# Optimization experiments

Measured on AMD Instinct MI355X. Metric: run time of the kernel, lower is better.

## Reference

```python
import jax, jax.numpy as jnp
import numpy as np

N = 50000       # nodes
E = 800000      # edges
H = 128         # hidden_channels
L = 5           # num_layers
EIN = 16        # edge_in_channels
G = 512         # graphs in batch
NODE_VOCAB = 100
BN_EPS = 1e-5


def setup_inputs() -> dict:
    key = jax.random.key(0)
    ks = jax.random.split(key, 12)
    s = 0.1  # init scale
    return {
        "x": jax.random.randint(ks[0], (N,), 0, NODE_VOCAB, dtype=jnp.int32),
        "edge_index": jax.random.randint(ks[1], (2, E), 0, N, dtype=jnp.int32),
        "edge_attr": jax.random.normal(ks[2], (E, EIN), jnp.float32),
        "batch": jnp.sort(jax.random.randint(ks[3], (N,), 0, G, dtype=jnp.int32)),
        "node_emb": jax.random.normal(ks[4], (NODE_VOCAB, H), jnp.float32) * s,
        "edge_W": jax.random.normal(ks[5], (L, EIN, H), jnp.float32) * s,
        "edge_b": jnp.zeros((L, H), jnp.float32),
        "eps": jnp.zeros((L,), jnp.float32),
        "W1": jax.random.normal(ks[6], (L, H, 2 * H), jnp.float32) * s,
        "b1": jnp.zeros((L, 2 * H), jnp.float32),
        "g1": jnp.ones((L, 2 * H), jnp.float32),
        "be1": jnp.zeros((L, 2 * H), jnp.float32),
        "W2": jax.random.normal(ks[7], (L, 2 * H, H), jnp.float32) * s,
        "b2": jnp.zeros((L, H), jnp.float32),
        "bn_g": jnp.ones((L, H), jnp.float32),
        "bn_b": jnp.zeros((L, H), jnp.float32),
        "out_W": jax.random.normal(ks[8], (H, H), jnp.float32) * s,
        "out_b": jnp.zeros((H,), jnp.float32),
    }


def _bn(h, gamma, beta):
    # training-mode BatchNorm1d: batch statistics over the node axis
    m = h.mean(0)
    v = jnp.mean((h - m) ** 2, axis=0)
    return (h - m) * jax.lax.rsqrt(v + BN_EPS) * gamma + beta


def reference(x, edge_index, edge_attr, batch, node_emb, edge_W, edge_b, eps,
              W1, b1, g1, be1, W2, b2, bn_g, bn_b, out_W, out_b):
    h = node_emb[x]                                   # [N,H] node encoder
    src, dst = edge_index[0], edge_index[1]
    for i in range(L):
        # EGINConv: edge encode, gather->relu->scatter-add, GIN MLP
        e = edge_attr @ edge_W[i] + edge_b[i]         # [E,H]
        msg = jax.nn.relu(h[src] + e)                 # gather + relu
        agg = jax.ops.segment_sum(msg, dst, num_segments=N)  # scatter-add
        z = (1.0 + eps[i]) * h + agg
        z = jax.nn.relu(_bn(z @ W1[i] + b1[i], g1[i], be1[i]))  # mlp inner
        h = _bn(z @ W2[i] + b2[i], bn_g[i], bn_b[i])  # inter-layer BN
        if i < L - 1:
            h = jax.nn.relu(h)                        # dropout: eval (identity)
    # global_mean_pool
    sums = jax.ops.segment_sum(h, batch, num_segments=G)
    cnt = jax.ops.segment_sum(jnp.ones((N, 1), h.dtype), batch, num_segments=G)
    pooled = sums / jnp.maximum(cnt, 1.0)
    return pooled @ out_W + out_b                     # [G,H]
```

## Files before the change

kernel.cpp:

```cpp
#include <hip/hip_runtime.h>
#include <hip/hip_fp16.h>

#define N_NODES 50000
#define N_EDGES 800000
#define HD 128
#define NLAYERS 5
#define EINC 16
#define NG 512

typedef _Float16 half8 __attribute__((ext_vector_type(8)));
typedef _Float16 half2v __attribute__((ext_vector_type(2)));
typedef float f32x4 __attribute__((ext_vector_type(4)));
typedef float f32x2 __attribute__((ext_vector_type(2)));

__global__ __launch_bounds__(256) void k_embed(const int* __restrict__ x,
                                               const float* __restrict__ emb,
                                               _Float16* __restrict__ h) {
  int i = blockIdx.x * 256 + threadIdx.x;
  if (i < N_NODES * 16) {
    int n = i >> 4, cv = i & 15;
    const float* src = &emb[(size_t)x[n] * HD + cv * 8];
    float4 a0 = *(const float4*)&src[0];
    float4 a1 = *(const float4*)&src[4];
    half8 p;
    p[0] = (_Float16)a0.x; p[1] = (_Float16)a0.y; p[2] = (_Float16)a0.z; p[3] = (_Float16)a0.w;
    p[4] = (_Float16)a1.x; p[5] = (_Float16)a1.y; p[6] = (_Float16)a1.z; p[7] = (_Float16)a1.w;
    *(half8*)&h[(size_t)n * HD + cv * 8] = p;
  }
}

__global__ __launch_bounds__(256) void k_hist(const int* __restrict__ ei,
                                              int* __restrict__ deg) {
  int e = blockIdx.x * 256 + threadIdx.x;
  if (e < N_EDGES) atomicAdd(&deg[ei[N_EDGES + e]], 1);
}

__global__ __launch_bounds__(256) void k_scan1(const int* __restrict__ deg,
                                               int* __restrict__ incl,
                                               int* __restrict__ bsum) {
  __shared__ int s[256];
  int i = blockIdx.x * 256 + threadIdx.x;
  int v = (i < N_NODES) ? deg[i] : 0;
  s[threadIdx.x] = v;
  __syncthreads();
  for (int d = 1; d < 256; d <<= 1) {
    int t = (threadIdx.x >= d) ? s[threadIdx.x - d] : 0;
    __syncthreads();
    s[threadIdx.x] += t;
    __syncthreads();
  }
  if (i < N_NODES) incl[i] = s[threadIdx.x];
  if (threadIdx.x == 255) bsum[blockIdx.x] = s[255];
}

__global__ void k_scan2(int* __restrict__ bsum, int nb) {
  __shared__ int s[256];
  int v = (threadIdx.x < nb) ? bsum[threadIdx.x] : 0;
  s[threadIdx.x] = v;
  __syncthreads();
  for (int d = 1; d < 256; d <<= 1) {
    int t = (threadIdx.x >= d) ? s[threadIdx.x - d] : 0;
    __syncthreads();
    s[threadIdx.x] += t;
    __syncthreads();
  }
  if (threadIdx.x < nb) bsum[threadIdx.x] = s[threadIdx.x];
}

__global__ __launch_bounds__(256) void k_scan3(const int* __restrict__ deg,
                                               const int* __restrict__ incl,
                                               const int* __restrict__ bsum,
                                               int* __restrict__ offs,
                                               int* __restrict__ cursor) {
  int i = blockIdx.x * 256 + threadIdx.x;
  if (i < N_NODES) {
    int base = (blockIdx.x > 0) ? bsum[blockIdx.x - 1] : 0;
    int start = base + incl[i] - deg[i];
    offs[i] = start;
    cursor[i] = start;
    if (i == N_NODES - 1) offs[N_NODES] = N_EDGES;
  }
}

__global__ __launch_bounds__(256) void k_scatter(const int* __restrict__ ei,
                                                 int* __restrict__ cursor,
                                                 int2* __restrict__ edata) {
  int e = blockIdx.x * 256 + threadIdx.x;
  if (e < N_EDGES) {
    int dst = ei[N_EDGES + e];
    int pos = atomicAdd(&cursor[dst], 1);
    edata[pos] = make_int2(ei[e], e);
  }
}

__global__ __launch_bounds__(256) void k_cvtw1(const float* __restrict__ W1,
                                               _Float16* __restrict__ w1t) {
  int i = blockIdx.x * 256 + threadIdx.x;
  if (i < NLAYERS * 256 * 128) {
    int l = i >> 15, r = i & 32767;
    int n = r >> 7, k = r & 127;
    w1t[i] = (_Float16)W1[(size_t)l * 32768 + k * 256 + n];
  }
}
__global__ __launch_bounds__(256) void k_cvtw2(const float* __restrict__ W2,
                                               _Float16* __restrict__ w2t) {
  int i = blockIdx.x * 256 + threadIdx.x;
  if (i < NLAYERS * 128 * 256) {
    int l = i >> 15, r = i & 32767;
    int n = r >> 8, k = r & 255;
    w2t[i] = (_Float16)W2[(size_t)l * 32768 + k * 128 + n];
  }
}

__global__ __launch_bounds__(256) void k_aggr(const int* __restrict__ offs,
                                              const int2* __restrict__ edata,
                                              const float* __restrict__ ea,
                                              const float* __restrict__ W,
                                              const float* __restrict__ eb,
                                              const float* __restrict__ epsA, int layer,
                                              const _Float16* __restrict__ hraw,
                                              const float* __restrict__ bnsc,
                                              const float* __restrict__ bnsh,
                                              int fuse_bn,
                                              _Float16* __restrict__ z) {
  const int wid = threadIdx.x >> 6;
  const int lane = threadIdx.x & 63;
  int n = blockIdx.x * 4 + wid;
  if (n >= N_NODES) return;
  const int c0 = lane * 2;

  f32x2 wp[EINC];
#pragma unroll
  for (int k = 0; k < EINC; ++k) wp[k] = *(const f32x2*)&W[k * HD + c0];
  const f32x2 ebp = *(const f32x2*)&eb[c0];
  const float epsv = 1.0f + epsA[layer];
  const f32x2 zero = {0.f, 0.f};
  f32x2 scp = {1.f, 1.f}, shp = {0.f, 0.f};
  if (fuse_bn) {
    scp = *(const f32x2*)&bnsc[c0];
    shp = *(const f32x2*)&bnsh[c0];
  }

  int j0 = offs[n], j1 = offs[n + 1];
  half2v hv = *(const half2v*)&hraw[(size_t)n * HD + c0];
  f32x2 hn; hn[0] = (float)hv[0]; hn[1] = (float)hv[1];
  if (fuse_bn) hn = __builtin_elementwise_max(__builtin_elementwise_fma(hn, scp, shp), zero);
  f32x2 acc;
  acc[0] = epsv * hn[0];
  acc[1] = epsv * hn[1];

  int j = j0;
  for (; j + 3 < j1; j += 4) {
    int2 d0 = edata[j], d1 = edata[j + 1], d2 = edata[j + 2], d3 = edata[j + 3];
    const float* r0 = &ea[(size_t)__builtin_amdgcn_readfirstlane(d0.y) * EINC];
    const float* r1 = &ea[(size_t)__builtin_amdgcn_readfirstlane(d1.y) * EINC];
    const float* r2 = &ea[(size_t)__builtin_amdgcn_readfirstlane(d2.y) * EINC];
    const float* r3 = &ea[(size_t)__builtin_amdgcn_readfirstlane(d3.y) * EINC];
    half2v v0h = *(const half2v*)&hraw[(size_t)d0.x * HD + c0];
    half2v v1h = *(const half2v*)&hraw[(size_t)d1.x * HD + c0];
    half2v v2h = *(const half2v*)&hraw[(size_t)d2.x * HD + c0];
    half2v v3h = *(const half2v*)&hraw[(size_t)d3.x * HD + c0];
    f32x2 g0, g1, g2, g3;
    g0[0] = (float)v0h[0]; g0[1] = (float)v0h[1];
    g1[0] = (float)v1h[0]; g1[1] = (float)v1h[1];
    g2[0] = (float)v2h[0]; g2[1] = (float)v2h[1];
    g3[0] = (float)v3h[0]; g3[1] = (float)v3h[1];
    if (fuse_bn) {
      g0 = __builtin_elementwise_max(__builtin_elementwise_fma(g0, scp, shp), zero);
      g1 = __builtin_elementwise_max(__builtin_elementwise_fma(g1, scp, shp), zero);
      g2 = __builtin_elementwise_max(__builtin_elementwise_fma(g2, scp, shp), zero);
      g3 = __builtin_elementwise_max(__builtin_elementwise_fma(g3, scp, shp), zero);
    }
    f32x2 e0 = ebp, e1 = ebp, e2 = ebp, e3 = ebp;
#pragma unroll
    for (int k = 0; k < EINC; ++k) {
      f32x2 w2 = wp[k];
      float a0 = r0[k], a1 = r1[k], a2 = r2[k], a3 = r3[k];
      f32x2 va0 = {a0, a0}, va1 = {a1, a1}, va2 = {a2, a2}, va3 = {a3, a3};
      e0 = __builtin_elementwise_fma(va0, w2, e0);
      e1 = __builtin_elementwise_fma(va1, w2, e1);
      e2 = __builtin_elementwise_fma(va2, w2, e2);
      e3 = __builtin_elementwise_fma(va3, w2, e3);
    }
    acc += __builtin_elementwise_max(g0 + e0, zero);
    acc += __builtin_elementwise_max(g1 + e1, zero);
    acc += __builtin_elementwise_max(g2 + e2, zero);
    acc += __builtin_elementwise_max(g3 + e3, zero);
  }
  for (; j < j1; ++j) {
    int2 d0 = edata[j];
    const float* r0 = &ea[(size_t)__builtin_amdgcn_readfirstlane(d0.y) * EINC];
    half2v v0h = *(const half2v*)&hraw[(size_t)d0.x * HD + c0];
    f32x2 g0; g0[0] = (float)v0h[0]; g0[1] = (float)v0h[1];
    if (fuse_bn) g0 = __builtin_elementwise_max(__builtin_elementwise_fma(g0, scp, shp), zero);
    f32x2 e0 = ebp;
#pragma unroll
    for (int k = 0; k < EINC; ++k) {
      float a0 = r0[k];
      f32x2 va0 = {a0, a0};
      e0 = __builtin_elementwise_fma(va0, wp[k], e0);
    }
    acc += __builtin_elementwise_max(g0 + e0, zero);
  }
  half2v oz; oz[0] = (_Float16)acc[0]; oz[1] = (_Float16)acc[1];
  *(half2v*)&z[(size_t)n * HD + c0] = oz;
}

__global__ __launch_bounds__(256) void k_gemm1m(const _Float16* __restrict__ z,
                                                const _Float16* __restrict__ w1t,
                                                const float* __restrict__ bias,
                                                _Float16* __restrict__ y1h,
                                                float* __restrict__ gsum,
                                                float* __restrict__ gsq) {
  __shared__ _Float16 sA[128 * 40];
  __shared__ _Float16 sBT[128 * 40];
  __shared__ float ssum[128], ssq[128];
  const int tid = threadIdx.x;
  const int lane = tid & 63;
  const int wid = tid >> 6;
  const int wm = wid >> 1, wn = wid & 1;
  const int m0 = blockIdx.x * 128;
  const int n0 = blockIdx.y * 128;

  if (tid < 128) { ssum[tid] = 0.f; ssq[tid] = 0.f; }

  f32x4 acc[4][4];
  const f32x4 zz = {0.f, 0.f, 0.f, 0.f};
#pragma unroll
  for (int a = 0; a < 4; ++a)
#pragma unroll
    for (int b = 0; b < 4; ++b) acc[a][b] = zz;

  const int srow = tid >> 1;
  const int skh = (tid & 1) * 16;

  for (int k0 = 0; k0 < 128; k0 += 32) {
    {
      int n = m0 + srow;
      half8 p0, p1;
      if (n < N_NODES) {
        p0 = *(const half8*)&z[(size_t)n * 128 + k0 + skh];
        p1 = *(const half8*)&z[(size_t)n * 128 + k0 + skh + 8];
      } else {
#pragma unroll
        for (int j = 0; j < 8; ++j) { p0[j] = (_Float16)0.f; p1[j] = (_Float16)0.f; }
      }
      *(half8*)&sA[srow * 40 + skh] = p0;
      *(half8*)&sA[srow * 40 + skh + 8] = p1;
    }
    {
      half8 u0 = *(const half8*)&w1t[(size_t)(n0 + srow) * 128 + k0 + skh];
      half8 u1 = *(const half8*)&w1t[(size_t)(n0 + srow) * 128 + k0 + skh + 8];
      *(half8*)&sBT[srow * 40 + skh] = u0;
      *(half8*)&sBT[srow * 40 + skh + 8] = u1;
    }
    __syncthreads();
    half8 af[4], bf[4];
#pragma unroll
    for (int t = 0; t < 4; ++t) {
      af[t] = *(const half8*)&sA[(wm * 64 + t * 16 + (lane & 15)) * 40 + (lane >> 4) * 8];
      bf[t] = *(const half8*)&sBT[(wn * 64 + t * 16 + (lane & 15)) * 40 + (lane >> 4) * 8];
    }
#pragma unroll
    for (int tm = 0; tm < 4; ++tm)
#pragma unroll
      for (int tn = 0; tn < 4; ++tn)
        acc[tm][tn] = __builtin_amdgcn_mfma_f32_16x16x32_f16(af[tm], bf[tn], acc[tm][tn], 0, 0, 0);
    __syncthreads();
  }

  float bsv[4];
#pragma unroll
  for (int tn = 0; tn < 4; ++tn) bsv[tn] = bias[n0 + wn * 64 + tn * 16 + (lane & 15)];
  float sacc[4] = {0.f, 0.f, 0.f, 0.f}, qacc[4] = {0.f, 0.f, 0.f, 0.f};
#pragma unroll
  for (int tm = 0; tm < 4; ++tm) {
    int nbase = m0 + wm * 64 + tm * 16 + (lane >> 4) * 4;
#pragma unroll
    for (int r = 0; r < 4; ++r) {
      int n = nbase + r;
      if (n < N_NODES) {
#pragma unroll
        for (int tn = 0; tn < 4; ++tn) {
          float v = acc[tm][tn][r] + bsv[tn];
          y1h[(size_t)n * 256 + n0 + wn * 64 + tn * 16 + (lane & 15)] = (_Float16)v;
          sacc[tn] += v; qacc[tn] += v * v;
        }
      }
    }
  }
#pragma unroll
  for (int tn = 0; tn < 4; ++tn) {
    int c = wn * 64 + tn * 16 + (lane & 15);
    atomicAdd(&ssum[c], sacc[tn]);
    atomicAdd(&ssq[c], qacc[tn]);
  }
  __syncthreads();
  if (tid < 128) {
    unsafeAtomicAdd(&gsum[n0 + tid], ssum[tid]);
    unsafeAtomicAdd(&gsq[n0 + tid], ssq[tid]);
  }
}

__global__ __launch_bounds__(256) void k_gemm2m(const _Float16* __restrict__ y1h,
                                                const float* __restrict__ sc,
                                                const float* __restrict__ sh,
                                                const _Float16* __restrict__ w2t,
                                                const float* __restrict__ bias,
                                                _Float16* __restrict__ y2,
                                                float* __restrict__ gsum,
                                                float* __restrict__ gsq) {
  __shared__ _Float16 sA[64 * 40];
  __shared__ _Float16 sBT[128 * 40];
  __shared__ float ssc[256], ssh[256];
  __shared__ float ssum[128], ssq[128];
  const int tid = threadIdx.x;
  const int lane = tid & 63;
  const int wid = tid >> 6;
  const int wm = wid >> 1, wn = wid & 1;
  const int m0 = blockIdx.x * 64;

  ssc[tid] = sc[tid];
  ssh[tid] = sh[tid];
  if (tid < 128) { ssum[tid] = 0.f; ssq[tid] = 0.f; }
  __syncthreads();

  f32x4 acc[2][4];
  const f32x4 zz = {0.f, 0.f, 0.f, 0.f};
#pragma unroll
  for (int a = 0; a < 2; ++a)
#pragma unroll
    for (int b = 0; b < 4; ++b) acc[a][b] = zz;

  const int arow = tid >> 2;
  const int akq = (tid & 3) * 8;
  const int brow = tid >> 1;
  const int bkh = (tid & 1) * 16;

  for (int k0 = 0; k0 < 256; k0 += 32) {
    {
      int n = m0 + arow;
      half8 p;
      if (n < N_NODES) {
        half8 yv = *(const half8*)&y1h[(size_t)n * 256 + k0 + akq];
#pragma unroll
        for (int j = 0; j < 8; ++j) {
          float v = fmaxf((float)yv[j] * ssc[k0 + akq + j] + ssh[k0 + akq + j], 0.f);
          p[j] = (_Float16)v;
        }
      } else {
#pragma unroll
        for (int j = 0; j < 8; ++j) p[j] = (_Float16)0.f;
      }
      *(half8*)&sA[arow * 40 + akq] = p;
    }
    {
      half8 u0 = *(const half8*)&w2t[(size_t)brow * 256 + k0 + bkh];
      half8 u1 = *(const half8*)&w2t[(size_t)brow * 256 + k0 + bkh + 8];
      *(half8*)&sBT[brow * 40 + bkh] = u0;
      *(half8*)&sBT[brow * 40 + bkh + 8] = u1;
    }
    __syncthreads();
    half8 af[2], bf[4];
#pragma unroll
    for (int t = 0; t < 2; ++t)
      af[t] = *(const half8*)&sA[(wm * 32 + t * 16 + (lane & 15)) * 40 + (lane >> 4) * 8];
#pragma unroll
    for (int t = 0; t < 4; ++t)
      bf[t] = *(const half8*)&sBT[(wn * 64 + t * 16 + (lane & 15)) * 40 + (lane >> 4) * 8];
#pragma unroll
    for (int tm = 0; tm < 2; ++tm)
#pragma unroll
      for (int tn = 0; tn < 4; ++tn)
        acc[tm][tn] = __builtin_amdgcn_mfma_f32_16x16x32_f16(af[tm], bf[tn], acc[tm][tn], 0, 0, 0);
    __syncthreads();
  }

  float bsv[4];
#pragma unroll
  for (int tn = 0; tn < 4; ++tn) bsv[tn] = bias[wn * 64 + tn * 16 + (lane & 15)];
  float sacc[4] = {0.f, 0.f, 0.f, 0.f}, qacc[4] = {0.f, 0.f, 0.f, 0.f};
#pragma unroll
  for (int tm = 0; tm < 2; ++tm) {
    int nbase = m0 + wm * 32 + tm * 16 + (lane >> 4) * 4;
#pragma unroll
    for (int r = 0; r < 4; ++r) {
      int n = nbase + r;
      if (n < N_NODES) {
#pragma unroll
        for (int tn = 0; tn < 4; ++tn) {
          float v = acc[tm][tn][r] + bsv[tn];
          y2[(size_t)n * 128 + wn * 64 + tn * 16 + (lane & 15)] = (_Float16)v;
          sacc[tn] += v; qacc[tn] += v * v;
        }
      }
    }
  }
#pragma unroll
  for (int tn = 0; tn < 4; ++tn) {
    int c = wn * 64 + tn * 16 + (lane & 15);
    atomicAdd(&ssum[c], sacc[tn]);
    atomicAdd(&ssq[c], qacc[tn]);
  }
  __syncthreads();
  if (tid < 128) {
    unsafeAtomicAdd(&gsum[tid], ssum[tid]);
    unsafeAtomicAdd(&gsq[tid], ssq[tid]);
  }
}

__global__ void k_bnfin(const float* __restrict__ sum, const float* __restrict__ sq,
                        const float* __restrict__ g, const float* __restrict__ b,
                        float* __restrict__ sc, float* __restrict__ sh, int C) {
  int c = blockIdx.x * blockDim.x + threadIdx.x;
  if (c < C) {
    const float invN = 1.0f / (float)N_NODES;
    float m = sum[c] * invN;
    float v = fmaxf(sq[c] * invN - m * m, 0.0f);
    float rs = rsqrtf(v + 1e-5f);
    float scale = g[c] * rs;
    sc[c] = scale;
    sh[c] = b[c] - m * scale;
  }
}

__global__ void k_goff(const int* __restrict__ batch, int* __restrict__ goff) {
  int g = blockIdx.x * blockDim.x + threadIdx.x;
  if (g <= NG) {
    if (g == NG) { goff[g] = N_NODES; return; }
    int lo = 0, hi = N_NODES;
    while (lo < hi) { int mid = (lo + hi) >> 1; if (batch[mid] < g) lo = mid + 1; else hi = mid; }
    goff[g] = lo;
  }
}

__global__ __launch_bounds__(256) void k_poolseg(const _Float16* __restrict__ y2raw,
                                                 const float* __restrict__ sc,
                                                 const float* __restrict__ sh,
                                                 const int* __restrict__ goff,
                                                 float* __restrict__ pooled) {
  __shared__ float sred[256];
  int g = blockIdx.x;
  int c = threadIdx.x & 127;
  int half = threadIdx.x >> 7;
  int n0 = goff[g], n1 = goff[g + 1];
  float s = 0.f;
  for (int n = n0 + half; n < n1; n += 2) s += (float)y2raw[(size_t)n * HD + c];
  sred[threadIdx.x] = s;
  __syncthreads();
  if (threadIdx.x < 128) {
    float tot = sred[threadIdx.x] + sred[threadIdx.x + 128];
    float cntf = fmaxf((float)(n1 - n0), 1.0f);
    pooled[g * HD + threadIdx.x] = sc[threadIdx.x] * (tot / cntf) + sh[threadIdx.x];
  }
}

__global__ __launch_bounds__(128) void k_final(const float* __restrict__ pooled,
                                               const float* __restrict__ oW,
                                               const float* __restrict__ ob,
                                               float* __restrict__ out) {
  __shared__ float sP[HD];
  int g = blockIdx.x;
  int c = threadIdx.x;
  sP[c] = pooled[g * HD + c];
  __syncthreads();
  float acc = ob[c];
#pragma unroll 8
  for (int k = 0; k < HD; ++k) acc += sP[k] * oW[k * HD + c];
  out[g * HD + c] = acc;
}

extern "C" void kernel_launch(void* const* d_in, const int* in_sizes, int n_in,
                              void* d_out, int out_size, void* d_ws, size_t ws_size,
                              hipStream_t stream) {
  const int* x = (const int*)d_in[0];
  const int* ei = (const int*)d_in[1];
  const float* ea = (const float*)d_in[2];
  const int* batch = (const int*)d_in[3];
  const float* emb = (const float*)d_in[4];
  const float* eW = (const float*)d_in[5];
  const float* eb = (const float*)d_in[6];
  const float* epsA = (const float*)d_in[7];
  const float* W1 = (const float*)d_in[8];
  const float* b1 = (const float*)d_in[9];
  const float* g1 = (const float*)d_in[10];
  const float* be1 = (const float*)d_in[11];
  const float* W2 = (const float*)d_in[12];
  const float* b2 = (const float*)d_in[13];
  const float* bng = (const float*)d_in[14];
  const float* bnb = (const float*)d_in[15];
  const float* oW = (const float*)d_in[16];
  const float* ob = (const float*)d_in[17];
  float* out = (float*)d_out;

  int* ip = (int*)d_ws;
  int* deg = ip;
  int* incl = deg + 50000;
  int* offs = incl + 50000;
  int* cursor = offs + 50001;
  int2* edata = (int2*)(cursor + 50000 + 1);
  int* bsum = (int*)(edata + 800000);
  int* goff = bsum + 200;
  float* fp = (float*)(ip + 1800916);
  _Float16* h = (_Float16*)fp;
  _Float16* zbuf = (_Float16*)(fp + 6400000);
  _Float16* y1h = (_Float16*)(fp + 12800000);
  float* stats = fp + 19200000;
  float* sc1 = stats + 768;
  float* sh1 = sc1 + 256;
  float* sc2 = sh1 + 256;
  float* sh2 = sc2 + 128;
  float* pooled = sh2 + 128;
  _Float16* w1t = (_Float16*)(pooled + 65536);
  _Float16* w2t = w1t + 163840;

  const int edge_blocks = (N_EDGES + 255) / 256;
  const int node_blocks = (N_NODES + 255) / 256;

  k_embed<<<(N_NODES * 16 + 255) / 256, 256, 0, stream>>>(x, emb, h);

  hipMemsetAsync(deg, 0, 50000 * sizeof(int), stream);
  k_hist<<<edge_blocks, 256, 0, stream>>>(ei, deg);
  k_scan1<<<node_blocks, 256, 0, stream>>>(deg, incl, bsum);
  k_scan2<<<1, 256, 0, stream>>>(bsum, node_blocks);
  k_scan3<<<node_blocks, 256, 0, stream>>>(deg, incl, bsum, offs, cursor);
  k_scatter<<<edge_blocks, 256, 0, stream>>>(ei, cursor, edata);
  k_goff<<<3, 256, 0, stream>>>(batch, goff);
  k_cvtw1<<<640, 256, 0, stream>>>(W1, w1t);
  k_cvtw2<<<640, 256, 0, stream>>>(W2, w2t);

  for (int l = 0; l < NLAYERS; ++l) {
    hipMemsetAsync(stats, 0, 768 * sizeof(float), stream);
    k_aggr<<<(N_NODES + 3) / 4, 256, 0, stream>>>(offs, edata, ea,
                                                  eW + (size_t)l * EINC * HD, eb + l * HD,
                                                  epsA, l, h, sc2, sh2, (l > 0) ? 1 : 0,
                                                  zbuf);
    k_gemm1m<<<dim3(391, 2), 256, 0, stream>>>(zbuf, w1t + (size_t)l * 32768,
                                               b1 + l * 256, y1h, stats, stats + 256);
    k_bnfin<<<1, 256, 0, stream>>>(stats, stats + 256, g1 + l * 256, be1 + l * 256, sc1, sh1, 256);
    k_gemm2m<<<782, 256, 0, stream>>>(y1h, sc1, sh1, w2t + (size_t)l * 32768,
                                      b2 + l * HD, h, stats + 512, stats + 640);
    k_bnfin<<<1, 128, 0, stream>>>(stats + 512, stats + 640, bng + l * HD, bnb + l * HD, sc2, sh2, 128);
  }

  k_poolseg<<<NG, 256, 0, stream>>>(h, sc2, sh2, goff, pooled);
  k_final<<<NG, 128, 0, stream>>>(pooled, oW, ob, out);
}
```

Measured before the change: 997.9 us.

## Presort edge attrs to CSR order in fp16, packed-half aggregation split over two waves

Adds a one-time pass that writes edge attributes in destination-sorted order as duplicated fp16 pairs and a contiguous source-index array, so the aggregation kernel reads them sequentially instead of by random edge id. The edge encoding, BN apply and relu now run in packed fp16 math, and each node's edge range is split across two wavefronts whose partial sums are combined through shared memory. The goal is cheaper per-edge loads and ALU work and more parallelism for high-degree nodes. In exchange it adds a 51 MB buffer write, a block-wide sync, and fp16 rounding of the edge projection and BN affine.

New measurement: 985.1 us. No clear change (-1.3%).

```diff
diff --git a/kernel.cpp b/kernel.cpp
--- a/kernel.cpp
+++ b/kernel.cpp
@@ -12,6 +12,8 @@
 typedef _Float16 half2v __attribute__((ext_vector_type(2)));
 typedef float f32x4 __attribute__((ext_vector_type(4)));
 typedef float f32x2 __attribute__((ext_vector_type(2)));
+
+__device__ inline half2v h2bc(uint32_t u) { return __builtin_bit_cast(half2v, u); }
 
 __global__ __launch_bounds__(256) void k_embed(const int* __restrict__ x,
                                                const float* __restrict__ emb,
@@ -93,6 +95,25 @@
   }
 }
 
+__global__ __launch_bounds__(256) void k_permea(const int2* __restrict__ edata,
+                                                const float* __restrict__ ea,
+                                                int* __restrict__ srcs,
+                                                uint32_t* __restrict__ ea_dup) {
+  int p = blockIdx.x * 256 + threadIdx.x;
+  if (p < N_EDGES) {
+    int2 d = edata[p];
+    srcs[p] = d.x;
+    const float* r = &ea[(size_t)d.y * EINC];
+    uint32_t* o = &ea_dup[(size_t)p * EINC];
+#pragma unroll
+    for (int k = 0; k < EINC; ++k) {
+      _Float16 v = (_Float16)r[k];
+      half2v dv; dv[0] = v; dv[1] = v;
+      o[k] = __builtin_bit_cast(uint32_t, dv);
+    }
+  }
+}
+
 __global__ __launch_bounds__(256) void k_cvtw1(const float* __restrict__ W1,
                                                _Float16* __restrict__ w1t) {
   int i = blockIdx.x * 256 + threadIdx.x;
@@ -111,11 +132,16 @@
     w2t[i] = (_Float16)W2[(size_t)l * 32768 + k * 128 + n];
   }
 }
+__global__ __launch_bounds__(256) void k_cvtwe(const float* __restrict__ eW,
+                                               _Float16* __restrict__ eWh) {
+  int i = blockIdx.x * 256 + threadIdx.x;
+  if (i < NLAYERS * EINC * HD) eWh[i] = (_Float16)eW[i];
+}
 
 __global__ __launch_bounds__(256) void k_aggr(const int* __restrict__ offs,
-                                              const int2* __restrict__ edata,
-                                              const float* __restrict__ ea,
-                                              const float* __restrict__ W,
+                                              const int* __restrict__ srcs,
+                                              const uint32_t* __restrict__ ea_dup,
+                                              const _Float16* __restrict__ eWh,
                                               const float* __restrict__ eb,
                                               const float* __restrict__ epsA, int layer,
                                               const _Float16* __restrict__ hraw,
@@ -123,87 +149,98 @@
                                               const float* __restrict__ bnsh,
                                               int fuse_bn,
                                               _Float16* __restrict__ z) {
-  const int wid = threadIdx.x >> 6;
+  __shared__ float sP[2 * HD];
+  const int w = threadIdx.x >> 6;
   const int lane = threadIdx.x & 63;
-  int n = blockIdx.x * 4 + wid;
-  if (n >= N_NODES) return;
+  const int nodeIdx = w >> 1, sub = w & 1;
+  const int n = blockIdx.x * 2 + nodeIdx;
   const int c0 = lane * 2;
 
-  f32x2 wp[EINC];
-#pragma unroll
-  for (int k = 0; k < EINC; ++k) wp[k] = *(const f32x2*)&W[k * HD + c0];
-  const f32x2 ebp = *(const f32x2*)&eb[c0];
+  half2v wph[EINC];
+#pragma unroll
+  for (int k = 0; k < EINC; ++k) wph[k] = *(const half2v*)&eWh[k * HD + c0];
+  half2v ebh; ebh[0] = (_Float16)eb[c0]; ebh[1] = (_Float16)eb[c0 + 1];
+  half2v hz; hz[0] = (_Float16)0.f; hz[1] = (_Float16)0.f;
+  half2v sch = hz, shh = hz;
+  if (fuse_bn) {
+    sch[0] = (_Float16)bnsc[c0]; sch[1] = (_Float16)bnsc[c0 + 1];
+    shh[0] = (_Float16)bnsh[c0]; shh[1] = (_Float16)bnsh[c0 + 1];
+  }
   const float epsv = 1.0f + epsA[layer];
-  const f32x2 zero = {0.f, 0.f};
-  f32x2 scp = {1.f, 1.f}, shp = {0.f, 0.f};
-  if (fuse_bn) {
-    scp = *(const f32x2*)&bnsc[c0];
-    shp = *(const f32x2*)&bnsh[c0];
-  }
-
-  int j0 = offs[n], j1 = offs[n + 1];
-  half2v hv = *(const half2v*)&hraw[(size_t)n * HD + c0];
-  f32x2 hn; hn[0] = (float)hv[0]; hn[1] = (float)hv[1];
-  if (fuse_bn) hn = __builtin_elementwise_max(__builtin_elementwise_fma(hn, scp, shp), zero);
-  f32x2 acc;
-  acc[0] = epsv * hn[0];
-  acc[1] = epsv * hn[1];
-
-  int j = j0;
-  for (; j + 3 < j1; j += 4) {
-    int2 d0 = edata[j], d1 = edata[j + 1], d2 = edata[j + 2], d3 = edata[j + 3];
-    const float* r0 = &ea[(size_t)__builtin_amdgcn_readfirstlane(d0.y) * EINC];
-    const float* r1 = &ea[(size_t)__builtin_amdgcn_readfirstlane(d1.y) * EINC];
-    const float* r2 = &ea[(size_t)__builtin_amdgcn_readfirstlane(d2.y) * EINC];
-    const float* r3 = &ea[(size_t)__builtin_amdgcn_readfirstlane(d3.y) * EINC];
-    half2v v0h = *(const half2v*)&hraw[(size_t)d0.x * HD + c0];
-    half2v v1h = *(const half2v*)&hraw[(size_t)d1.x * HD + c0];
-    half2v v2h = *(const half2v*)&hraw[(size_t)d2.x * HD + c0];
-    half2v v3h = *(const half2v*)&hraw[(size_t)d3.x * HD + c0];
-    f32x2 g0, g1, g2, g3;
-    g0[0] = (float)v0h[0]; g0[1] = (float)v0h[1];
-    g1[0] = (float)v1h[0]; g1[1] = (float)v1h[1];
-    g2[0] = (float)v2h[0]; g2[1] = (float)v2h[1];
-    g3[0] = (float)v3h[0]; g3[1] = (float)v3h[1];
-    if (fuse_bn) {
-      g0 = __builtin_elementwise_max(__builtin_elementwise_fma(g0, scp, shp), zero);
-      g1 = __builtin_elementwise_max(__builtin_elementwise_fma(g1, scp, shp), zero);
-      g2 = __builtin_elementwise_max(__builtin_elementwise_fma(g2, scp, shp), zero);
-      g3 = __builtin_elementwise_max(__builtin_elementwise_fma(g3, scp, shp), zero);
-    }
-    f32x2 e0 = ebp, e1 = ebp, e2 = ebp, e3 = ebp;
-#pragma unroll
-    for (int k = 0; k < EINC; ++k) {
-      f32x2 w2 = wp[k];
-      float a0 = r0[k], a1 = r1[k], a2 = r2[k], a3 = r3[k];
-      f32x2 va0 = {a0, a0}, va1 = {a1, a1}, va2 = {a2, a2}, va3 = {a3, a3};
-      e0 = __builtin_elementwise_fma(va0, w2, e0);
-      e1 = __builtin_elementwise_fma(va1, w2, e1);
-      e2 = __builtin_elementwise_fma(va2, w2, e2);
-      e3 = __builtin_elementwise_fma(va3, w2, e3);
-    }
-    acc += __builtin_elementwise_max(g0 + e0, zero);
-    acc += __builtin_elementwise_max(g1 + e1, zero);
-    acc += __builtin_elementwise_max(g2 + e2, zero);
-    acc += __builtin_elementwise_max(g3 + e3, zero);
-  }
-  for (; j < j1; ++j) {
-    int2 d0 = edata[j];
-    const float* r0 = &ea[(size_t)__builtin_amdgcn_readfirstlane(d0.y) * EINC];
-    half2v v0h = *(const half2v*)&hraw[(size_t)d0.x * HD + c0];
-    f32x2 g0; g0[0] = (float)v0h[0]; g0[1] = (float)v0h[1];
-    if (fuse_bn) g0 = __builtin_elementwise_max(__builtin_elementwise_fma(g0, scp, shp), zero);
-    f32x2 e0 = ebp;
-#pragma unroll
-    for (int k = 0; k < EINC; ++k) {
-      float a0 = r0[k];
-      f32x2 va0 = {a0, a0};
-      e0 = __builtin_elementwise_fma(va0, wp[k], e0);
-    }
-    acc += __builtin_elementwise_max(g0 + e0, zero);
-  }
-  half2v oz; oz[0] = (_Float16)acc[0]; oz[1] = (_Float16)acc[1];
-  *(half2v*)&z[(size_t)n * HD + c0] = oz;
+
+  f32x2 acc = {0.f, 0.f};
+  if (n < N_NODES) {
+    int j0 = offs[n], j1 = offs[n + 1];
+    int jm = j0 + ((j1 - j0 + 1) >> 1);
+    int ja = sub ? jm : j0;
+    int jb = sub ? j1 : jm;
+
+    int jj = ja;
+    for (; jj + 3 < jb; jj += 4) {
+      int ju = __builtin_amdgcn_readfirstlane(jj);
+      const int* sj = &srcs[ju];
+      int s0 = sj[0], s1 = sj[1], s2 = sj[2], s3 = sj[3];
+      const uint32_t* ra = &ea_dup[(size_t)ju * EINC];
+      half2v g0 = *(const half2v*)&hraw[(size_t)s0 * HD + c0];
+      half2v g1 = *(const half2v*)&hraw[(size_t)s1 * HD + c0];
+      half2v g2 = *(const half2v*)&hraw[(size_t)s2 * HD + c0];
+      half2v g3 = *(const half2v*)&hraw[(size_t)s3 * HD + c0];
+      half2v e0 = ebh, e1 = ebh, e2 = ebh, e3 = ebh;
+#pragma unroll
+      for (int k = 0; k < EINC; ++k) {
+        half2v w2 = wph[k];
+        e0 = __builtin_elementwise_fma(h2bc(ra[k]), w2, e0);
+        e1 = __builtin_elementwise_fma(h2bc(ra[EINC + k]), w2, e1);
+        e2 = __builtin_elementwise_fma(h2bc(ra[2 * EINC + k]), w2, e2);
+        e3 = __builtin_elementwise_fma(h2bc(ra[3 * EINC + k]), w2, e3);
+      }
+      if (fuse_bn) {
+        g0 = __builtin_elementwise_max(__builtin_elementwise_fma(g0, sch, shh), hz);
+        g1 = __builtin_elementwise_max(__builtin_elementwise_fma(g1, sch, shh), hz);
+        g2 = __builtin_elementwise_max(__builtin_elementwise_fma(g2, sch, shh), hz);
+        g3 = __builtin_elementwise_max(__builtin_elementwise_fma(g3, sch, shh), hz);
+      }
+      half2v m0 = __builtin_elementwise_max(g0 + e0, hz);
+      half2v m1 = __builtin_elementwise_max(g1 + e1, hz);
+      half2v m2 = __builtin_elementwise_max(g2 + e2, hz);
+      half2v m3 = __builtin_elementwise_max(g3 + e3, hz);
+      acc[0] += (float)m0[0]; acc[1] += (float)m0[1];
+      acc[0] += (float)m1[0]; acc[1] += (float)m1[1];
+      acc[0] += (float)m2[0]; acc[1] += (float)m2[1];
+      acc[0] += (float)m3[0]; acc[1] += (float)m3[1];
+    }
+    for (; jj < jb; ++jj) {
+      int ju = __builtin_amdgcn_readfirstlane(jj);
+      int s0 = srcs[ju];
+      const uint32_t* ra = &ea_dup[(size_t)ju * EINC];
+      half2v g0 = *(const half2v*)&hraw[(size_t)s0 * HD + c0];
+      half2v e0 = ebh;
+#pragma unroll
+      for (int k = 0; k < EINC; ++k)
+        e0 = __builtin_elementwise_fma(h2bc(ra[k]), wph[k], e0);
+      if (fuse_bn)
+        g0 = __builtin_elementwise_max(__builtin_elementwise_fma(g0, sch, shh), hz);
+      half2v m0 = __builtin_elementwise_max(g0 + e0, hz);
+      acc[0] += (float)m0[0]; acc[1] += (float)m0[1];
+    }
+
+    if (!sub) {
+      half2v hv = *(const half2v*)&hraw[(size_t)n * HD + c0];
+      if (fuse_bn) hv = __builtin_elementwise_max(__builtin_elementwise_fma(hv, sch, shh), hz);
+      acc[0] += epsv * (float)hv[0];
+      acc[1] += epsv * (float)hv[1];
+    } else {
+      sP[nodeIdx * HD + c0] = acc[0];
+      sP[nodeIdx * HD + c0 + 1] = acc[1];
+    }
+  }
+  __syncthreads();
+  if (n < N_NODES && !sub) {
+    acc[0] += sP[nodeIdx * HD + c0];
+    acc[1] += sP[nodeIdx * HD + c0 + 1];
+    half2v oz; oz[0] = (_Float16)acc[0]; oz[1] = (_Float16)acc[1];
+    *(half2v*)&z[(size_t)n * HD + c0] = oz;
+  }
 }
 
 __global__ __launch_bounds__(256) void k_gemm1m(const _Float16* __restrict__ z,
@@ -499,13 +536,15 @@
   int* offs = incl + 50000;
   int* cursor = offs + 50001;
   int2* edata = (int2*)(cursor + 50000 + 1);
-  int* bsum = (int*)(edata + 800000);
+  int* srcs = (int*)(edata + 800000);
+  int* bsum = srcs + 800000;
   int* goff = bsum + 200;
-  float* fp = (float*)(ip + 1800916);
+  float* fp = (float*)(ip + 2600716);
   _Float16* h = (_Float16*)fp;
-  _Float16* zbuf = (_Float16*)(fp + 6400000);
-  _Float16* y1h = (_Float16*)(fp + 12800000);
-  float* stats = fp + 19200000;
+  _Float16* zbuf = (_Float16*)(fp + 3200000);
+  _Float16* y1h = (_Float16*)(fp + 6400000);
+  uint32_t* ea_dup = (uint32_t*)(fp + 12800000);
+  float* stats = fp + 25600000;
   float* sc1 = stats + 768;
   float* sh1 = sc1 + 256;
   float* sc2 = sh1 + 256;
@@ -513,6 +552,7 @@
   float* pooled = sh2 + 128;
   _Float16* w1t = (_Float16*)(pooled + 65536);
   _Float16* w2t = w1t + 163840;
+  _Float16* eWh = w2t + 163840;
 
   const int edge_blocks = (N_EDGES + 255) / 256;
   const int node_blocks = (N_NODES + 255) / 256;
@@ -525,14 +565,16 @@
   k_scan2<<<1, 256, 0, stream>>>(bsum, node_blocks);
   k_scan3<<<node_blocks, 256, 0, stream>>>(deg, incl, bsum, offs, cursor);
   k_scatter<<<edge_blocks, 256, 0, stream>>>(ei, cursor, edata);
+  k_permea<<<edge_blocks, 256, 0, stream>>>(edata, ea, srcs, ea_dup);
   k_goff<<<3, 256, 0, stream>>>(batch, goff);
   k_cvtw1<<<640, 256, 0, stream>>>(W1, w1t);
   k_cvtw2<<<640, 256, 0, stream>>>(W2, w2t);
+  k_cvtwe<<<(NLAYERS * EINC * HD + 255) / 256, 256, 0, stream>>>(eW, eWh);
 
   for (int l = 0; l < NLAYERS; ++l) {
     hipMemsetAsync(stats, 0, 768 * sizeof(float), stream);
-    k_aggr<<<(N_NODES + 3) / 4, 256, 0, stream>>>(offs, edata, ea,
-                                                  eW + (size_t)l * EINC * HD, eb + l * HD,
+    k_aggr<<<(N_NODES + 1) / 2, 256, 0, stream>>>(offs, srcs, ea_dup,
+                                                  eWh + (size_t)l * EINC * HD, eb + l * HD,
                                                   epsA, l, h, sc2, sh2, (l > 0) ? 1 : 0,
                                                   zbuf);
     k_gemm1m<<<dim3(391, 2), 256, 0, stream>>>(zbuf, w1t + (size_t)l * 32768,
```
